# Kernel optimization log

Hardware: AMD Instinct MI355X
Metric: run time of the kernel (lower is better)

The kernel has to match this reference:

```python
import jax, jax.numpy as jnp
import numpy as np

ITERS = 3          # num_iterations
EPS_ATTN = 1e-8    # epsilon offset on attention
LN_EPS = 1e-5      # torch LayerNorm default eps


def _ln(x, g, b):
    m = x.mean(-1, keepdims=True)
    v = ((x - m) ** 2).mean(-1, keepdims=True)
    return (x - m) * jax.lax.rsqrt(v + LN_EPS) * g + b


def setup_inputs() -> dict:
    key = jax.random.key(0)
    ks = jax.random.split(key, 16)
    B, N, D, S, H = 64, 4096, 64, 8, 128

    def lin_w(k, fan_in, fan_out):
        lim = (1.0 / fan_in) ** 0.5
        return jax.random.uniform(k, (fan_in, fan_out), minval=-lim, maxval=lim, dtype=jnp.float32)

    def lin_b(k, fan_in, fan_out):
        lim = (1.0 / fan_in) ** 0.5
        return jax.random.uniform(k, (fan_out,), minval=-lim, maxval=lim, dtype=jnp.float32)

    return {
        "inputs": jax.random.normal(ks[0], (B, N, D), dtype=jnp.float32),
        "noise": jax.random.normal(ks[1], (B, S, D), dtype=jnp.float32),
        "slots_mu": jax.random.normal(ks[2], (1, 1, D), dtype=jnp.float32),
        "slots_log_sigma": jax.random.uniform(ks[3], (1, 1, D), minval=-0.3, maxval=0.3, dtype=jnp.float32),
        "wq": lin_w(ks[4], D, D), "bq": lin_b(ks[4], D, D),
        "wk": lin_w(ks[5], D, D), "bk": lin_b(ks[5], D, D),
        "wv": lin_w(ks[6], D, D), "bv": lin_b(ks[6], D, D),
        "w_ih": lin_w(ks[7], D, 3 * D), "b_ih": lin_b(ks[7], D, 3 * D),
        "w_hh": lin_w(ks[8], D, 3 * D), "b_hh": lin_b(ks[8], D, 3 * D),
        "w1": lin_w(ks[9], D, H), "b1": lin_b(ks[9], D, H),
        "w2": lin_w(ks[10], H, D), "b2": lin_b(ks[10], H, D),
        "g_in": jnp.ones((D,), jnp.float32), "beta_in": jnp.zeros((D,), jnp.float32),
        "g_sl": jnp.ones((D,), jnp.float32), "beta_sl": jnp.zeros((D,), jnp.float32),
        "g_ff": jnp.ones((D,), jnp.float32), "beta_ff": jnp.zeros((D,), jnp.float32),
    }


def reference(inputs, noise, slots_mu, slots_log_sigma, wq, bq, wk, bk, wv, bv,
              w_ih, b_ih, w_hh, b_hh, w1, b1, w2, b2,
              g_in, beta_in, g_sl, beta_sl, g_ff, beta_ff):
    b, n, d = inputs.shape
    scale = d ** -0.5

    slots = slots_mu + jnp.exp(slots_log_sigma) * noise          # [b, S, d]
    x = _ln(inputs, g_in, beta_in)
    k = x @ wk + bk                                              # [b, n, d]
    v = x @ wv + bv                                              # [b, n, d]

    for _ in range(ITERS):
        slots_prev = slots
        q = _ln(slots, g_sl, beta_sl) @ wq + bq                  # [b, S, d]
        dots = jnp.einsum('bid,bjd->bij', q, k) * scale          # [b, S, n]
        attn = jax.nn.softmax(dots, axis=1) + EPS_ATTN           # softmax over slots
        attn = attn / attn.sum(-1, keepdims=True)                # renorm over inputs
        updates = jnp.einsum('bjd,bij->bid', v, attn)            # [b, S, d]

        # GRUCell (torch gate order: reset, update, new)
        gx = updates @ w_ih + b_ih
        gh = slots_prev @ w_hh + b_hh
        xr, xz, xn = jnp.split(gx, 3, axis=-1)
        hr, hz, hn = jnp.split(gh, 3, axis=-1)
        r = jax.nn.sigmoid(xr + hr)
        z = jax.nn.sigmoid(xz + hz)
        nw = jnp.tanh(xn + r * hn)
        slots = (1.0 - z) * nw + z * slots_prev

        # residual MLP
        ff = _ln(slots, g_ff, beta_ff)
        slots = slots + (jax.nn.relu(ff @ w1 + b1) @ w2 + b2)
    return slots
```

## Files before the change

kernel.cpp:

```cpp
#include <hip/hip_runtime.h>
#include <math.h>

#define LN_EPS 1e-5f
#define EPS_ATTN 1e-8f
#define SCALE 0.125f
#define CHUNKS 32

__device__ __forceinline__ float wsum64(float v) {
#pragma unroll
  for (int m = 1; m <= 32; m <<= 1) v += __shfl_xor(v, m, 64);
  return v;
}

__device__ __forceinline__ float red16(float v) {
  v += __int_as_float(__builtin_amdgcn_update_dpp(0, __float_as_int(v), 0xB1, 0xF, 0xF, true));
  v += __int_as_float(__builtin_amdgcn_update_dpp(0, __float_as_int(v), 0x4E, 0xF, 0xF, true));
  v += __int_as_float(__builtin_amdgcn_update_dpp(0, __float_as_int(v), 0x124, 0xF, 0xF, true));
  v += __int_as_float(__builtin_amdgcn_update_dpp(0, __float_as_int(v), 0x128, 0xF, 0xF, true));
  return v;
}

__global__ __launch_bounds__(256) void k_prep(
    const float* __restrict__ wq, const float* __restrict__ wk,
    const float* __restrict__ bq, const float* __restrict__ bk,
    float* __restrict__ M, float* __restrict__ cvec,
    float* __restrict__ uvec, float* __restrict__ s0v)
{
  __shared__ float wqs[64 * 64];
  __shared__ float wks[64 * 65];
  int tid = threadIdx.x;
  for (int i = tid; i < 4096; i += 256) wqs[i] = wq[i];
  for (int i = tid; i < 4096; i += 256) wks[(i >> 6) * 65 + (i & 63)] = wk[i];
  __syncthreads();

  int idx = blockIdx.x * 256 + tid;
  int t = idx >> 6, d = idx & 63;
  float a = 0.0f;
#pragma unroll 8
  for (int j = 0; j < 64; ++j) a += wqs[t * 64 + j] * wks[d * 65 + j];
  M[idx] = a * SCALE;

  if (blockIdx.x == 0) {
    if (tid < 64) {
      float cc = 0.0f;
#pragma unroll 8
      for (int j = 0; j < 64; ++j) cc += bq[j] * wks[tid * 65 + j];
      cvec[tid] = cc * SCALE;
    } else if (tid < 128) {
      int t2 = tid - 64;
      float uu = 0.0f;
#pragma unroll 8
      for (int j = 0; j < 64; ++j) uu += wqs[t2 * 64 + j] * bk[j];
      uvec[t2] = uu * SCALE;
    } else if (tid == 128) {
      float ss = 0.0f;
      for (int j = 0; j < 64; ++j) ss += bq[j] * bk[j];
      s0v[0] = ss * SCALE;
    }
  }
}

__device__ void slot_qk_wave(int bi, float o, int lane,
    const float* __restrict__ M, const float* __restrict__ cvec,
    const float* __restrict__ uvec, const float* __restrict__ s0v,
    const float* __restrict__ g_sl, const float* __restrict__ beta_sl,
    float* __restrict__ qk, float* __restrict__ qb)
{
  float s  = wsum64(o);
  float s2 = wsum64(o * o);
  float mean = s * (1.0f / 64.0f);
  float var  = s2 * (1.0f / 64.0f) - mean * mean;
  float rstd = rsqrtf(var + LN_EPS);
  float ln = (o - mean) * rstd * g_sl[lane] + beta_sl[lane];

  float qv = cvec[lane];
#pragma unroll
  for (int t = 0; t < 64; ++t) qv += __shfl(ln, t, 64) * M[t * 64 + lane];
  qk[bi * 64 + lane] = qv;
  float pb = wsum64(ln * uvec[lane]);
  if (lane == 0) qb[bi] = s0v[0] + pb;
}

__device__ void slot_update_wave(int bi, int lane, int do_next,
    const float* __restrict__ S_in, float* __restrict__ S_out,
    float* __restrict__ acc, float* __restrict__ asum,
    const float* __restrict__ wv, const float* __restrict__ bv,
    const float* __restrict__ w_ih, const float* __restrict__ b_ih,
    const float* __restrict__ w_hh, const float* __restrict__ b_hh,
    const float* __restrict__ w1, const float* __restrict__ b1,
    const float* __restrict__ w2, const float* __restrict__ b2,
    const float* __restrict__ g_ff, const float* __restrict__ beta_ff,
    const float* __restrict__ M, const float* __restrict__ cvec,
    const float* __restrict__ uvec, const float* __restrict__ s0v,
    const float* __restrict__ g_sl, const float* __restrict__ beta_sl,
    float* __restrict__ qk, float* __restrict__ qb)
{
  float asv = asum[bi];
  float av  = acc[bi * 64 + lane];
  float v   = av / asv;
  if (do_next) {
    acc[bi * 64 + lane] = 0.0f;
    if (lane == 0) asum[bi] = 0.0f;
  }
  float sp = S_in[bi * 64 + lane];

  float upd = bv[lane];
#pragma unroll
  for (int e = 0; e < 64; ++e) upd += __shfl(v, e, 64) * wv[e * 64 + lane];

  float gxr = b_ih[lane], gxz = b_ih[64 + lane], gxn = b_ih[128 + lane];
  float ghr = b_hh[lane], ghz = b_hh[64 + lane], ghn = b_hh[128 + lane];
#pragma unroll 16
  for (int e = 0; e < 64; ++e) {
    float uu = __shfl(upd, e, 64), hh = __shfl(sp, e, 64);
    const float* wi = w_ih + e * 192;
    const float* wh = w_hh + e * 192;
    gxr += uu * wi[lane]; gxz += uu * wi[64 + lane]; gxn += uu * wi[128 + lane];
    ghr += hh * wh[lane]; ghz += hh * wh[64 + lane]; ghn += hh * wh[128 + lane];
  }
  float r  = 1.0f / (1.0f + __expf(-(gxr + ghr)));
  float z  = 1.0f / (1.0f + __expf(-(gxz + ghz)));
  float nw = tanhf(gxn + r * ghn);
  float sn = (1.0f - z) * nw + z * sp;

  float s  = wsum64(sn);
  float s2 = wsum64(sn * sn);
  float mean = s * (1.0f / 64.0f);
  float var  = s2 * (1.0f / 64.0f) - mean * mean;
  float rstd = rsqrtf(var + LN_EPS);
  float ff = (sn - mean) * rstd * g_ff[lane] + beta_ff[lane];

  float h1 = b1[lane], h2 = b1[64 + lane];
#pragma unroll
  for (int e = 0; e < 64; ++e) {
    float f = __shfl(ff, e, 64);
    h1 += f * w1[e * 128 + lane];
    h2 += f * w1[e * 128 + 64 + lane];
  }
  h1 = fmaxf(h1, 0.0f);
  h2 = fmaxf(h2, 0.0f);

  float o = sn + b2[lane];
#pragma unroll
  for (int t = 0; t < 64; ++t) o += __shfl(h1, t, 64) * w2[t * 64 + lane];
#pragma unroll
  for (int t = 0; t < 64; ++t) o += __shfl(h2, t, 64) * w2[(64 + t) * 64 + lane];

  S_out[bi * 64 + lane] = o;

  if (do_next)
    slot_qk_wave(bi, o, lane, M, cvec, uvec, s0v, g_sl, beta_sl, qk, qb);
}

__global__ __launch_bounds__(64) void k_init(
    const float* __restrict__ noise, const float* __restrict__ mu,
    const float* __restrict__ lsig,
    const float* __restrict__ M, const float* __restrict__ cvec,
    const float* __restrict__ uvec, const float* __restrict__ s0v,
    const float* __restrict__ g_sl, const float* __restrict__ beta_sl,
    float* __restrict__ S_buf, float* __restrict__ qk, float* __restrict__ qb,
    float* __restrict__ acc, float* __restrict__ asum)
{
  int bi = blockIdx.x;
  int lane = threadIdx.x;
  float sl = mu[lane] + __expf(lsig[lane]) * noise[bi * 64 + lane];
  S_buf[bi * 64 + lane] = sl;
  acc[bi * 64 + lane] = 0.0f;
  if (lane == 0) asum[bi] = 0.0f;
  slot_qk_wave(bi, sl, lane, M, cvec, uvec, s0v, g_sl, beta_sl, qk, qb);
}

__global__ __launch_bounds__(64) void k_update(
    const float* __restrict__ S_in, float* __restrict__ S_out,
    float* __restrict__ acc, float* __restrict__ asum,
    const float* __restrict__ wv, const float* __restrict__ bv,
    const float* __restrict__ w_ih, const float* __restrict__ b_ih,
    const float* __restrict__ w_hh, const float* __restrict__ b_hh,
    const float* __restrict__ w1, const float* __restrict__ b1,
    const float* __restrict__ w2, const float* __restrict__ b2,
    const float* __restrict__ g_ff, const float* __restrict__ beta_ff,
    const float* __restrict__ M, const float* __restrict__ cvec,
    const float* __restrict__ uvec, const float* __restrict__ s0v,
    const float* __restrict__ g_sl, const float* __restrict__ beta_sl,
    float* __restrict__ qk, float* __restrict__ qb, int do_next)
{
  slot_update_wave(blockIdx.x, threadIdx.x, do_next,
                   S_in, S_out, acc, asum, wv, bv, w_ih, b_ih, w_hh, b_hh,
                   w1, b1, w2, b2, g_ff, beta_ff, M, cvec, uvec, s0v,
                   g_sl, beta_sl, qk, qb);
}

__global__ __launch_bounds__(256) void k_main(
    const float* __restrict__ inputs,
    const float* __restrict__ g_in, const float* __restrict__ beta_in,
    const float* __restrict__ qk, const float* __restrict__ qb,
    float* __restrict__ acc, float* __restrict__ asum)
{
  __shared__ float lds_acc[4][512];
  __shared__ float lds_as[4][8];
  const int b = blockIdx.y;
  const int chunk = blockIdx.x;
  const int tid = threadIdx.x;
  const int lane = tid & 63;
  const int wave = tid >> 6;
  const int p = lane & 15;

  float4 g4  = ((const float4*)g_in)[p];
  float4 be4 = ((const float4*)beta_in)[p];
  float4 qkv[8];
  float qbv[8];
  const float4* qk4 = (const float4*)(qk + b * 512);
#pragma unroll
  for (int i = 0; i < 8; ++i) {
    qkv[i] = qk4[i * 16 + p];
    qbv[i] = qb[b * 8 + i];
  }

  float4 accl[8];
  float asl[8];
#pragma unroll
  for (int i = 0; i < 8; ++i) { accl[i] = make_float4(0.f, 0.f, 0.f, 0.f); asl[i] = 0.f; }

  const float4* in4 = (const float4*)(inputs + (size_t)b * 4096 * 64);
  const int rb0 = chunk * 128 + wave * 4;

  float4 xv = in4[rb0 * 16 + lane];
  for (int it = 0; it < 8; ++it) {
    float4 nxt;
    if (it < 7) nxt = in4[(rb0 + (it + 1) * 16) * 16 + lane];

    float s  = red16(xv.x + xv.y + xv.z + xv.w);
    float s2 = red16(xv.x * xv.x + xv.y * xv.y + xv.z * xv.z + xv.w * xv.w);
    float mean = s * 0.015625f;
    float var  = s2 * 0.015625f - mean * mean;
    float rstd = rsqrtf(var + LN_EPS);
    float4 xln;
    xln.x = (xv.x - mean) * rstd * g4.x + be4.x;
    xln.y = (xv.y - mean) * rstd * g4.y + be4.y;
    xln.z = (xv.z - mean) * rstd * g4.z + be4.z;
    xln.w = (xv.w - mean) * rstd * g4.w + be4.w;

    float dots[8];
#pragma unroll
    for (int i = 0; i < 8; ++i) {
      float d = xln.x * qkv[i].x + xln.y * qkv[i].y + xln.z * qkv[i].z + xln.w * qkv[i].w;
      dots[i] = red16(d) + qbv[i];
    }

    float mx = dots[0];
#pragma unroll
    for (int i = 1; i < 8; ++i) mx = fmaxf(mx, dots[i]);
    float pv[8];
    float ps = 0.0f;
#pragma unroll
    for (int i = 0; i < 8; ++i) { pv[i] = __expf(dots[i] - mx); ps += pv[i]; }
    float inv = __builtin_amdgcn_rcpf(ps);
#pragma unroll
    for (int i = 0; i < 8; ++i) {
      float pp = pv[i] * inv + EPS_ATTN;
      asl[i] += pp;
      accl[i].x += pp * xln.x;
      accl[i].y += pp * xln.y;
      accl[i].z += pp * xln.z;
      accl[i].w += pp * xln.w;
    }
    xv = nxt;
  }

#pragma unroll
  for (int i = 0; i < 8; ++i) {
#pragma unroll
    for (int m = 16; m <= 32; m <<= 1) {
      accl[i].x += __shfl_xor(accl[i].x, m, 64);
      accl[i].y += __shfl_xor(accl[i].y, m, 64);
      accl[i].z += __shfl_xor(accl[i].z, m, 64);
      accl[i].w += __shfl_xor(accl[i].w, m, 64);
      asl[i]    += __shfl_xor(asl[i], m, 64);
    }
  }

  if (lane < 16) {
    float4* dst = (float4*)lds_acc[wave];
#pragma unroll
    for (int i = 0; i < 8; ++i) dst[i * 16 + p] = accl[i];
  }
  if (lane == 0) {
#pragma unroll
    for (int i = 0; i < 8; ++i) lds_as[wave][i] = asl[i];
  }
  __syncthreads();

  for (int f = tid; f < 512; f += 256) {
    float ssum = lds_acc[0][f] + lds_acc[1][f] + lds_acc[2][f] + lds_acc[3][f];
    atomicAdd(&acc[b * 512 + f], ssum);
  }
  if (tid < 8) {
    float ssum = lds_as[0][tid] + lds_as[1][tid] + lds_as[2][tid] + lds_as[3][tid];
    atomicAdd(&asum[b * 8 + tid], ssum);
  }
}

extern "C" void kernel_launch(void* const* d_in, const int* in_sizes, int n_in,
                              void* d_out, int out_size, void* d_ws, size_t ws_size,
                              hipStream_t stream) {
  const float* inputs  = (const float*)d_in[0];
  const float* noise   = (const float*)d_in[1];
  const float* mu      = (const float*)d_in[2];
  const float* lsig    = (const float*)d_in[3];
  const float* wq      = (const float*)d_in[4];
  const float* bq      = (const float*)d_in[5];
  const float* wk      = (const float*)d_in[6];
  const float* bk      = (const float*)d_in[7];
  const float* wv      = (const float*)d_in[8];
  const float* bv      = (const float*)d_in[9];
  const float* w_ih    = (const float*)d_in[10];
  const float* b_ih    = (const float*)d_in[11];
  const float* w_hh    = (const float*)d_in[12];
  const float* b_hh    = (const float*)d_in[13];
  const float* w1      = (const float*)d_in[14];
  const float* b1      = (const float*)d_in[15];
  const float* w2      = (const float*)d_in[16];
  const float* b2      = (const float*)d_in[17];
  const float* g_in    = (const float*)d_in[18];
  const float* beta_in = (const float*)d_in[19];
  const float* g_sl    = (const float*)d_in[20];
  const float* beta_sl = (const float*)d_in[21];
  const float* g_ff    = (const float*)d_in[22];
  const float* beta_ff = (const float*)d_in[23];

  float* S_buf = (float*)d_ws;
  float* qk    = S_buf + 32768;
  float* qb    = qk + 32768;
  float* acc   = qb + 512;
  float* asum  = acc + 32768;
  float* M     = asum + 512;
  float* cvec  = M + 4096;
  float* uvec  = cvec + 64;
  float* s0v   = uvec + 64;
  float* out   = (float*)d_out;

  k_prep<<<16, 256, 0, stream>>>(wq, wk, bq, bk, M, cvec, uvec, s0v);
  k_init<<<512, 64, 0, stream>>>(noise, mu, lsig, M, cvec, uvec, s0v,
                                 g_sl, beta_sl, S_buf, qk, qb, acc, asum);

  for (int t = 0; t < 3; ++t) {
    k_main<<<dim3(CHUNKS, 64), 256, 0, stream>>>(inputs, g_in, beta_in,
                                                 qk, qb, acc, asum);
    float* dst = (t == 2) ? out : S_buf;
    k_update<<<512, 64, 0, stream>>>(S_buf, dst, acc, asum, wv, bv,
                                     w_ih, b_ih, w_hh, b_hh, w1, b1, w2, b2,
                                     g_ff, beta_ff, M, cvec, uvec, s0v,
                                     g_sl, beta_sl, qk, qb, (t == 2) ? 0 : 1);
  }
}
```

Before: 243.0 us.

## Merge prep into init kernel and process two rows per iteration in main

Drops the separate k_prep launch. Its M, cvec, uvec and s0v products are now computed by extra blocks of k_init, and the initial q·k for the slots is computed directly from wq and wk. The main kernel halves the chunk count, so each wave handles two row groups per iteration with two loads in flight, which gives more independent work per wave at the cost of fewer blocks. The softmax max-subtraction is removed. This saves instructions but risks overflow in exp if the dot products are large.

```diff
diff --git a/kernel.cpp b/kernel.cpp
--- a/kernel.cpp
+++ b/kernel.cpp
@@ -4,7 +4,7 @@
 #define LN_EPS 1e-5f
 #define EPS_ATTN 1e-8f
 #define SCALE 0.125f
-#define CHUNKS 32
+#define CHUNKS 16
 
 __device__ __forceinline__ float wsum64(float v) {
 #pragma unroll
@@ -18,46 +18,6 @@
   v += __int_as_float(__builtin_amdgcn_update_dpp(0, __float_as_int(v), 0x124, 0xF, 0xF, true));
   v += __int_as_float(__builtin_amdgcn_update_dpp(0, __float_as_int(v), 0x128, 0xF, 0xF, true));
   return v;
-}
-
-__global__ __launch_bounds__(256) void k_prep(
-    const float* __restrict__ wq, const float* __restrict__ wk,
-    const float* __restrict__ bq, const float* __restrict__ bk,
-    float* __restrict__ M, float* __restrict__ cvec,
-    float* __restrict__ uvec, float* __restrict__ s0v)
-{
-  __shared__ float wqs[64 * 64];
-  __shared__ float wks[64 * 65];
-  int tid = threadIdx.x;
-  for (int i = tid; i < 4096; i += 256) wqs[i] = wq[i];
-  for (int i = tid; i < 4096; i += 256) wks[(i >> 6) * 65 + (i & 63)] = wk[i];
-  __syncthreads();
-
-  int idx = blockIdx.x * 256 + tid;
-  int t = idx >> 6, d = idx & 63;
-  float a = 0.0f;
-#pragma unroll 8
-  for (int j = 0; j < 64; ++j) a += wqs[t * 64 + j] * wks[d * 65 + j];
-  M[idx] = a * SCALE;
-
-  if (blockIdx.x == 0) {
-    if (tid < 64) {
-      float cc = 0.0f;
-#pragma unroll 8
-      for (int j = 0; j < 64; ++j) cc += bq[j] * wks[tid * 65 + j];
-      cvec[tid] = cc * SCALE;
-    } else if (tid < 128) {
-      int t2 = tid - 64;
-      float uu = 0.0f;
-#pragma unroll 8
-      for (int j = 0; j < 64; ++j) uu += wqs[t2 * 64 + j] * bk[j];
-      uvec[t2] = uu * SCALE;
-    } else if (tid == 128) {
-      float ss = 0.0f;
-      for (int j = 0; j < 64; ++j) ss += bq[j] * bk[j];
-      s0v[0] = ss * SCALE;
-    }
-  }
 }
 
 __device__ void slot_qk_wave(int bi, float o, int lane,
@@ -155,19 +115,56 @@
 __global__ __launch_bounds__(64) void k_init(
     const float* __restrict__ noise, const float* __restrict__ mu,
     const float* __restrict__ lsig,
-    const float* __restrict__ M, const float* __restrict__ cvec,
-    const float* __restrict__ uvec, const float* __restrict__ s0v,
+    const float* __restrict__ wq, const float* __restrict__ bq,
+    const float* __restrict__ wk, const float* __restrict__ bk,
     const float* __restrict__ g_sl, const float* __restrict__ beta_sl,
     float* __restrict__ S_buf, float* __restrict__ qk, float* __restrict__ qb,
-    float* __restrict__ acc, float* __restrict__ asum)
+    float* __restrict__ acc, float* __restrict__ asum,
+    float* __restrict__ M, float* __restrict__ cvec,
+    float* __restrict__ uvec, float* __restrict__ s0v)
 {
   int bi = blockIdx.x;
   int lane = threadIdx.x;
-  float sl = mu[lane] + __expf(lsig[lane]) * noise[bi * 64 + lane];
-  S_buf[bi * 64 + lane] = sl;
-  acc[bi * 64 + lane] = 0.0f;
-  if (lane == 0) asum[bi] = 0.0f;
-  slot_qk_wave(bi, sl, lane, M, cvec, uvec, s0v, g_sl, beta_sl, qk, qb);
+  if (bi < 512) {
+    float sl = mu[lane] + __expf(lsig[lane]) * noise[bi * 64 + lane];
+    S_buf[bi * 64 + lane] = sl;
+    acc[bi * 64 + lane] = 0.0f;
+    if (lane == 0) asum[bi] = 0.0f;
+
+    float s  = wsum64(sl);
+    float s2 = wsum64(sl * sl);
+    float mean = s * (1.0f / 64.0f);
+    float var  = s2 * (1.0f / 64.0f) - mean * mean;
+    float rstd = rsqrtf(var + LN_EPS);
+    float ln = (sl - mean) * rstd * g_sl[lane] + beta_sl[lane];
+
+    float q = bq[lane];
+#pragma unroll
+    for (int t = 0; t < 64; ++t) q += __shfl(ln, t, 64) * wq[t * 64 + lane];
+    float qkl = 0.0f;
+#pragma unroll
+    for (int d = 0; d < 64; ++d) qkl += __shfl(q, d, 64) * wk[lane * 64 + d];
+    qk[bi * 64 + lane] = qkl * SCALE;
+    float qbl = wsum64(q * bk[lane]);
+    if (lane == 0) qb[bi] = qbl * SCALE;
+  } else if (bi < 576) {
+    int t = bi - 512;
+    float wqv = wq[t * 64 + lane];
+    float m = 0.0f;
+#pragma unroll
+    for (int d = 0; d < 64; ++d) m += __shfl(wqv, d, 64) * wk[lane * 64 + d];
+    M[t * 64 + lane] = m * SCALE;
+    float uv = wsum64(wqv * bk[lane]);
+    if (lane == 0) uvec[t] = uv * SCALE;
+  } else {
+    float bqv = bq[lane];
+    float cc = 0.0f;
+#pragma unroll
+    for (int j = 0; j < 64; ++j) cc += __shfl(bqv, j, 64) * wk[lane * 64 + j];
+    cvec[lane] = cc * SCALE;
+    float ss = wsum64(bq[lane] * bk[lane]);
+    if (lane == 0) s0v[0] = ss * SCALE;
+  }
 }
 
 __global__ __launch_bounds__(64) void k_update(
@@ -222,49 +219,83 @@
   for (int i = 0; i < 8; ++i) { accl[i] = make_float4(0.f, 0.f, 0.f, 0.f); asl[i] = 0.f; }
 
   const float4* in4 = (const float4*)(inputs + (size_t)b * 4096 * 64);
-  const int rb0 = chunk * 128 + wave * 4;
-
-  float4 xv = in4[rb0 * 16 + lane];
+  const int rb0 = chunk * 256 + wave * 8;
+
+  float4 xa = in4[rb0 * 16 + lane];
+  float4 xb = in4[(rb0 + 4) * 16 + lane];
   for (int it = 0; it < 8; ++it) {
-    float4 nxt;
-    if (it < 7) nxt = in4[(rb0 + (it + 1) * 16) * 16 + lane];
-
-    float s  = red16(xv.x + xv.y + xv.z + xv.w);
-    float s2 = red16(xv.x * xv.x + xv.y * xv.y + xv.z * xv.z + xv.w * xv.w);
-    float mean = s * 0.015625f;
-    float var  = s2 * 0.015625f - mean * mean;
-    float rstd = rsqrtf(var + LN_EPS);
-    float4 xln;
-    xln.x = (xv.x - mean) * rstd * g4.x + be4.x;
-    xln.y = (xv.y - mean) * rstd * g4.y + be4.y;
-    xln.z = (xv.z - mean) * rstd * g4.z + be4.z;
-    xln.w = (xv.w - mean) * rstd * g4.w + be4.w;
-
-    float dots[8];
-#pragma unroll
-    for (int i = 0; i < 8; ++i) {
-      float d = xln.x * qkv[i].x + xln.y * qkv[i].y + xln.z * qkv[i].z + xln.w * qkv[i].w;
-      dots[i] = red16(d) + qbv[i];
+    float4 na, nb;
+    if (it < 7) {
+      na = in4[(rb0 + (it + 1) * 32) * 16 + lane];
+      nb = in4[(rb0 + (it + 1) * 32 + 4) * 16 + lane];
     }
 
-    float mx = dots[0];
-#pragma unroll
-    for (int i = 1; i < 8; ++i) mx = fmaxf(mx, dots[i]);
-    float pv[8];
-    float ps = 0.0f;
-#pragma unroll
-    for (int i = 0; i < 8; ++i) { pv[i] = __expf(dots[i] - mx); ps += pv[i]; }
-    float inv = __builtin_amdgcn_rcpf(ps);
-#pragma unroll
-    for (int i = 0; i < 8; ++i) {
-      float pp = pv[i] * inv + EPS_ATTN;
-      asl[i] += pp;
-      accl[i].x += pp * xln.x;
-      accl[i].y += pp * xln.y;
-      accl[i].z += pp * xln.z;
-      accl[i].w += pp * xln.w;
+    {
+      float s  = red16(xa.x + xa.y + xa.z + xa.w);
+      float s2 = red16(xa.x * xa.x + xa.y * xa.y + xa.z * xa.z + xa.w * xa.w);
+      float mean = s * 0.015625f;
+      float var  = s2 * 0.015625f - mean * mean;
+      float rstd = rsqrtf(var + LN_EPS);
+      float4 xln;
+      xln.x = (xa.x - mean) * rstd * g4.x + be4.x;
+      xln.y = (xa.y - mean) * rstd * g4.y + be4.y;
+      xln.z = (xa.z - mean) * rstd * g4.z + be4.z;
+      xln.w = (xa.w - mean) * rstd * g4.w + be4.w;
+      float dots[8];
+#pragma unroll
+      for (int i = 0; i < 8; ++i) {
+        float d = xln.x * qkv[i].x + xln.y * qkv[i].y + xln.z * qkv[i].z + xln.w * qkv[i].w;
+        dots[i] = red16(d) + qbv[i];
+      }
+      float pv[8];
+      float ps = 0.0f;
+#pragma unroll
+      for (int i = 0; i < 8; ++i) { pv[i] = __expf(dots[i]); ps += pv[i]; }
+      float inv = __builtin_amdgcn_rcpf(ps);
+#pragma unroll
+      for (int i = 0; i < 8; ++i) {
+        float pp = pv[i] * inv + EPS_ATTN;
+        asl[i] += pp;
+        accl[i].x += pp * xln.x;
+        accl[i].y += pp * xln.y;
+        accl[i].z += pp * xln.z;
+        accl[i].w += pp * xln.w;
+      }
     }
-    xv = nxt;
+    {
+      float s  = red16(xb.x + xb.y + xb.z + xb.w);
+      float s2 = red16(xb.x * xb.x + xb.y * xb.y + xb.z * xb.z + xb.w * xb.w);
+      float mean = s * 0.015625f;
+      float var  = s2 * 0.015625f - mean * mean;
+      float rstd = rsqrtf(var + LN_EPS);
+      float4 xln;
+      xln.x = (xb.x - mean) * rstd * g4.x + be4.x;
+      xln.y = (xb.y - mean) * rstd * g4.y + be4.y;
+      xln.z = (xb.z - mean) * rstd * g4.z + be4.z;
+      xln.w = (xb.w - mean) * rstd * g4.w + be4.w;
+      float dots[8];
+#pragma unroll
+      for (int i = 0; i < 8; ++i) {
+        float d = xln.x * qkv[i].x + xln.y * qkv[i].y + xln.z * qkv[i].z + xln.w * qkv[i].w;
+        dots[i] = red16(d) + qbv[i];
+      }
+      float pv[8];
+      float ps = 0.0f;
+#pragma unroll
+      for (int i = 0; i < 8; ++i) { pv[i] = __expf(dots[i]); ps += pv[i]; }
+      float inv = __builtin_amdgcn_rcpf(ps);
+#pragma unroll
+      for (int i = 0; i < 8; ++i) {
+        float pp = pv[i] * inv + EPS_ATTN;
+        asl[i] += pp;
+        accl[i].x += pp * xln.x;
+        accl[i].y += pp * xln.y;
+        accl[i].z += pp * xln.z;
+        accl[i].w += pp * xln.w;
+      }
+    }
+    xa = na;
+    xb = nb;
   }
 
 #pragma unroll
@@ -339,9 +370,9 @@
   float* s0v   = uvec + 64;
   float* out   = (float*)d_out;
 
-  k_prep<<<16, 256, 0, stream>>>(wq, wk, bq, bk, M, cvec, uvec, s0v);
-  k_init<<<512, 64, 0, stream>>>(noise, mu, lsig, M, cvec, uvec, s0v,
-                                 g_sl, beta_sl, S_buf, qk, qb, acc, asum);
+  k_init<<<577, 64, 0, stream>>>(noise, mu, lsig, wq, bq, wk, bk,
+                                 g_sl, beta_sl, S_buf, qk, qb, acc, asum,
+                                 M, cvec, uvec, s0v);
 
   for (int t = 0; t < 3; ++t) {
     k_main<<<dim3(CHUNKS, 64), 256, 0, stream>>>(inputs, g_in, beta_in,
```

After: 229.5 us. 5.5% less time.
